# Kernel optimization log

Hardware: AMD Instinct MI355X
Metric: run time of the kernel (lower is better)

The kernel has to match this reference:

```python
import jax, jax.numpy as jnp
import numpy as np

B, IN, OUT = 8192, 1024, 1024


def setup_inputs() -> dict:
    key = jax.random.key(0)
    k1, k2 = jax.random.split(key)
    x = jax.random.normal(k1, (B, IN), dtype=jnp.float32)
    W_seed = jax.random.normal(k2, (IN, OUT), dtype=jnp.float32) / np.sqrt(IN).astype(np.float32)
    b_seed = jnp.zeros((OUT,), dtype=jnp.float32)
    W_sig = jnp.zeros((2,), dtype=jnp.float32)  # mixture logits over ['dense','Toeplitz']
    b_sig = jnp.zeros((2,), dtype=jnp.float32)  # mixture logits over ['dense','None']
    A_sig = jnp.zeros((2,), dtype=jnp.float32)  # mixture logits over ['linear','relu']
    return {"x": x, "W_seed": W_seed, "b_seed": b_seed,
            "W_sig": W_sig, "b_sig": b_sig, "A_sig": A_sig}


def _toeplitz_from_seed(W_seed):
    # seed_vec = [W_seed[0, out-1], ..., W_seed[0, 1], W_seed[0,0], ..., W_seed[in-1,0]]
    in_sz, out_sz = W_seed.shape
    seed_vec = jnp.concatenate([W_seed[0, -1:0:-1], W_seed[:, 0]])  # [out-1 + in]
    # W_toep[i, j] = seed_vec[i - j + out - 1]
    idx = jnp.arange(in_sz)[:, None] - jnp.arange(out_sz)[None, :] + (out_sz - 1)
    return seed_vec[idx]  # [in, out]


def reference(x, W_seed, b_seed, W_sig, b_sig, A_sig):
    W_toep = _toeplitz_from_seed(W_seed)
    w_s = jax.nn.softmax(W_sig)
    W_core = w_s[0] * W_seed + w_s[1] * W_toep          # softmax-weighted weight mixture
    b_s = jax.nn.softmax(b_sig)
    b_core = b_s[0] * b_seed                             # 'None' branch contributes zeros
    out = x @ W_core + b_core                            # [B, out]
    a_s = jax.nn.softmax(A_sig)
    return a_s[0] * out + a_s[1] * jax.nn.relu(out)      # activation mixture
```

## Files before the change

### kernel.cpp

```cpp
#include <hip/hip_runtime.h>

typedef unsigned short ushort_t;
typedef __bf16 bf16x8 __attribute__((ext_vector_type(8)));
typedef float f32x4 __attribute__((ext_vector_type(4)));

#define AS1 __attribute__((address_space(1)))
#define AS3 __attribute__((address_space(3)))

__device__ __forceinline__ ushort_t f2bf(float f) {
    unsigned u = __builtin_bit_cast(unsigned, f);
    u = (u + 0x7fffu + ((u >> 16) & 1u)) >> 16;
    return (ushort_t)u;
}

__device__ __forceinline__ void async16(void* lds, const void* g) {
    __builtin_amdgcn_global_load_lds((const AS1 unsigned int*)g,
                                     (AS3 unsigned int*)lds, 16, 0, 0);
}

__device__ __forceinline__ void softmax2(const float* __restrict__ sig, float& s0, float& s1) {
    float a = sig[0], b = sig[1];
    float m = fmaxf(a, b);
    float e0 = __expf(a - m), e1 = __expf(b - m);
    float inv = 1.0f / (e0 + e1);
    s0 = e0 * inv; s1 = e1 * inv;
}

__device__ __forceinline__ float toep_val(const float* __restrict__ Wseed, int k, int o) {
    return (k >= o) ? Wseed[(size_t)(k - o) << 10] : Wseed[o - k];
}

__global__ __launch_bounds__(256) void prep_w_kernel(const float* __restrict__ Wseed,
                                                     const float* __restrict__ Wsig,
                                                     ushort_t* __restrict__ Wt) {
    __shared__ float T[64][65];
    int bb = blockIdx.x;
    int k0 = (bb >> 4) * 64;
    int o0 = (bb & 15) * 64;
    int t = threadIdx.x;
    #pragma unroll
    for (int i = 0; i < 4; ++i) {
        int lin = t + i * 256;
        int kr = lin >> 4;
        int c4 = lin & 15;
        float4 v = *(const float4*)&Wseed[(size_t)(k0 + kr) * 1024 + o0 + c4 * 4];
        T[kr][c4 * 4 + 0] = v.x;
        T[kr][c4 * 4 + 1] = v.y;
        T[kr][c4 * 4 + 2] = v.z;
        T[kr][c4 * 4 + 3] = v.w;
    }
    __syncthreads();
    float s0, s1; softmax2(Wsig, s0, s1);
    #pragma unroll
    for (int i = 0; i < 2; ++i) {
        int lin = t + i * 256;
        int oo = lin >> 3;
        int kq = (lin & 7) * 8;
        unsigned r[4];
        #pragma unroll
        for (int q = 0; q < 4; ++q) {
            float v0 = s0 * T[kq + 2 * q + 0][oo] + s1 * toep_val(Wseed, k0 + kq + 2 * q + 0, o0 + oo);
            float v1 = s0 * T[kq + 2 * q + 1][oo] + s1 * toep_val(Wseed, k0 + kq + 2 * q + 1, o0 + oo);
            r[q] = (unsigned)f2bf(v0) | ((unsigned)f2bf(v1) << 16);
        }
        *(uint4*)&Wt[(size_t)(o0 + oo) * 1024 + k0 + kq] = make_uint4(r[0], r[1], r[2], r[3]);
    }
}

#define BM 128
#define BN 128
#define BK 32
#define NKT 32

__global__ __launch_bounds__(512, 2) void gemm_kernel(const float* __restrict__ Xf,
                                                      const ushort_t* __restrict__ Wt,
                                                      const float* __restrict__ bseed,
                                                      const float* __restrict__ bsig,
                                                      const float* __restrict__ asig,
                                                      float* __restrict__ out) {
    __shared__ ushort_t lds[24576];
    ushort_t* At0 = lds;
    ushort_t* Bt0 = lds + 8192;
    ushort_t* At1 = lds + 12288;
    ushort_t* Bt1 = lds + 20480;

    const int t = threadIdx.x;
    const int wv = t >> 6;
    const int lane = t & 63;

    const int orig = blockIdx.x;
    const int g = orig & 7;
    const int within = orig >> 3;
    const int rb = g * 8 + (within >> 3);
    const int cb = within & 7;
    const int brow = rb * BM;
    const int bcol = cb * BN;

    const int ra = t >> 3;
    const int ca = (t & 7) ^ (ra & 7);
    const float* gAsw = Xf + (size_t)(brow + ra) * 1024 + 4 * ca;

    const int rbb = t >> 2;
    const int cbk = (t & 3) ^ (rbb & 3);
    const ushort_t* gBsw = Wt + (size_t)(bcol + rbb) * 1024 + 8 * cbk;

    f32x4 acc[2][4];
    #pragma unroll
    for (int i = 0; i < 2; ++i)
        #pragma unroll
        for (int j = 0; j < 4; ++j) acc[i][j] = (f32x4){0.f, 0.f, 0.f, 0.f};

    const int wr = (wv >> 1) * 32;
    const int wcn = (wv & 1) * 64;
    const int fr = lane & 15;
    const int kg = (lane >> 4) * 8;
    const int c0 = (lane >> 4) * 2;

    float bs0, bs1, as0, as1;
    softmax2(bsig, bs0, bs1);
    softmax2(asig, as0, as1);
    float bias[4];
    #pragma unroll
    for (int ni = 0; ni < 4; ++ni)
        bias[ni] = bs0 * bseed[bcol + wcn + ni * 16 + fr];
    asm volatile("" :: "v"(bias[0]), "v"(bias[1]), "v"(bias[2]), "v"(bias[3]),
                       "v"(as0), "v"(as1));
    asm volatile("" ::: "memory");

#define STAGEA(Abuf, ko)                                           \
    do {                                                           \
        async16((Abuf) + wv * 512,        gAsw + (ko));            \
        async16((Abuf) + 4096 + wv * 512, gAsw + 65536 + (ko));    \
    } while (0)

#define STAGEB(Bbuf, ko)                                   \
    do {                                                   \
        async16((Bbuf) + wv * 512, gBsw + (ko));           \
    } while (0)

#define COMPUTE(Abuf, Bbuf)                                                        \
    do {                                                                           \
        const float* Af_ = (const float*)(Abuf);                                   \
        bf16x8 af[2], bf[4];                                                       \
        _Pragma("unroll")                                                          \
        for (int mi = 0; mi < 2; ++mi) {                                           \
            int row_ = wr + mi * 16 + fr;                                          \
            f32x4 lo_ = *(const f32x4*)&Af_[row_ * 32 + (((c0)     ^ (row_ & 7)) << 2)]; \
            f32x4 hi_ = *(const f32x4*)&Af_[row_ * 32 + (((c0 + 1) ^ (row_ & 7)) << 2)]; \
            bf16x8 a_;                                                             \
            _Pragma("unroll")                                                      \
            for (int j_ = 0; j_ < 4; ++j_) {                                       \
                a_[j_]     = (__bf16)lo_[j_];                                      \
                a_[4 + j_] = (__bf16)hi_[j_];                                      \
            }                                                                      \
            af[mi] = a_;                                                           \
        }                                                                          \
        _Pragma("unroll")                                                          \
        for (int ni = 0; ni < 4; ++ni) {                                           \
            int rb_ = wcn + ni * 16 + fr;                                          \
            int ch_ = ((kg >> 3) ^ (rb_ & 3)) << 3;                                \
            bf[ni] = *(const bf16x8*)&(Bbuf)[rb_ * 32 + ch_];                      \
        }                                                                          \
        _Pragma("unroll")                                                          \
        for (int mi = 0; mi < 2; ++mi)                                             \
            _Pragma("unroll")                                                      \
            for (int ni = 0; ni < 4; ++ni)                                         \
                acc[mi][ni] = __builtin_amdgcn_mfma_f32_16x16x32_bf16(             \
                    af[mi], bf[ni], acc[mi][ni], 0, 0, 0);                         \
    } while (0)

#define SYNC() do { asm volatile("s_waitcnt vmcnt(0) lgkmcnt(0)" ::: "memory");    \
                    __builtin_amdgcn_s_barrier(); } while (0)

    STAGEA(At0, 0);
    STAGEB(Bt0, 0);
    SYNC();
    for (int it = 0; it < 15; ++it) {
        STAGEA(At1, (2 * it + 1) * BK);
        STAGEB(Bt1, (2 * it + 1) * BK);
        COMPUTE(At0, Bt0);
        SYNC();
        STAGEA(At0, (2 * it + 2) * BK);
        STAGEB(Bt0, (2 * it + 2) * BK);
        COMPUTE(At1, Bt1);
        SYNC();
    }
    STAGEA(At1, 31 * BK);
    STAGEB(Bt1, 31 * BK);
    COMPUTE(At0, Bt0);
    SYNC();
    COMPUTE(At1, Bt1);

    #pragma unroll
    for (int ni = 0; ni < 4; ++ni) {
        int col = bcol + wcn + ni * 16 + fr;
        #pragma unroll
        for (int mi = 0; mi < 2; ++mi) {
            int row = brow + wr + mi * 16 + (lane >> 4) * 4;
            #pragma unroll
            for (int r = 0; r < 4; ++r) {
                float v = acc[mi][ni][r] + bias[ni];
                out[(size_t)(row + r) * 1024 + col] = as0 * v + as1 * fmaxf(v, 0.f);
            }
        }
    }
#undef STAGEA
#undef STAGEB
#undef COMPUTE
#undef SYNC
}

__global__ __launch_bounds__(256) void naive_kernel(const float* __restrict__ x,
                                                    const float* __restrict__ Wseed,
                                                    const float* __restrict__ bseed,
                                                    const float* __restrict__ Wsig,
                                                    const float* __restrict__ bsig,
                                                    const float* __restrict__ asig,
                                                    float* __restrict__ out) {
    int idx = blockIdx.x * 256 + threadIdx.x;
    int b = idx >> 10, o = idx & 1023;
    float ws0, ws1, bs0, bs1, as0, as1;
    softmax2(Wsig, ws0, ws1);
    softmax2(bsig, bs0, bs1);
    softmax2(asig, as0, as1);
    float s = 0.f;
    const float* xr = x + (size_t)b * 1024;
    for (int k = 0; k < 1024; ++k) {
        float wc = ws0 * Wseed[((size_t)k << 10) + o] + ws1 * toep_val(Wseed, k, o);
        s += xr[k] * wc;
    }
    float v = s + bs0 * bseed[o];
    out[idx] = as0 * v + as1 * fmaxf(v, 0.f);
}

extern "C" void kernel_launch(void* const* d_in, const int* in_sizes, int n_in,
                              void* d_out, int out_size, void* d_ws, size_t ws_size,
                              hipStream_t stream) {
    const float* x     = (const float*)d_in[0];
    const float* Wseed = (const float*)d_in[1];
    const float* bseed = (const float*)d_in[2];
    const float* Wsig  = (const float*)d_in[3];
    const float* bsig  = (const float*)d_in[4];
    const float* Asig  = (const float*)d_in[5];
    float* out = (float*)d_out;

    const size_t need = (2u << 20) + 1024;
    if (ws_size < need) {
        naive_kernel<<<dim3(8192 * 1024 / 256), dim3(256), 0, stream>>>(
            x, Wseed, bseed, Wsig, bsig, Asig, out);
        return;
    }

    ushort_t* Wt = (ushort_t*)d_ws;

    prep_w_kernel<<<dim3(256), dim3(256), 0, stream>>>(Wseed, Wsig, Wt);
    gemm_kernel<<<dim3(512), dim3(512), 0, stream>>>(x, Wt, bseed, bsig, Asig, out);
}
```

Before: 38.84 us.

## Use triple-buffered LDS pipeline with partial vmcnt waits in GEMM

Replaces the double-buffered A/B staging with a three-stage rotating LDS buffer, so loads for tile T+2 are issued while tile T is computed. Waits use a partial vmcnt so only the oldest stage must land before each barrier. The B-tile XOR swizzle now keys on (row>>1) to change the LDS bank pattern, and the launch bounds request 4 blocks per CU. The risks are higher LDS use (72KB per block), which limits occupancy, and register pressure under the tighter launch bound.

New measurement: 39.18 us. About the same (+0.9%).

```diff
diff --git a/kernel.cpp b/kernel.cpp
--- a/kernel.cpp
+++ b/kernel.cpp
@@ -72,17 +72,16 @@
 #define BK 32
 #define NKT 32
 
-__global__ __launch_bounds__(512, 2) void gemm_kernel(const float* __restrict__ Xf,
+__global__ __launch_bounds__(512, 4) void gemm_kernel(const float* __restrict__ Xf,
                                                       const ushort_t* __restrict__ Wt,
                                                       const float* __restrict__ bseed,
                                                       const float* __restrict__ bsig,
                                                       const float* __restrict__ asig,
                                                       float* __restrict__ out) {
-    __shared__ ushort_t lds[24576];
-    ushort_t* At0 = lds;
-    ushort_t* Bt0 = lds + 8192;
-    ushort_t* At1 = lds + 12288;
-    ushort_t* Bt1 = lds + 20480;
+    __shared__ ushort_t lds[36864];
+    ushort_t* p0 = lds;
+    ushort_t* p1 = lds + 12288;
+    ushort_t* p2 = lds + 24576;
 
     const int t = threadIdx.x;
     const int wv = t >> 6;
@@ -101,7 +100,7 @@
     const float* gAsw = Xf + (size_t)(brow + ra) * 1024 + 4 * ca;
 
     const int rbb = t >> 2;
-    const int cbk = (t & 3) ^ (rbb & 3);
+    const int cbk = (t & 3) ^ ((rbb >> 1) & 3);
     const ushort_t* gBsw = Wt + (size_t)(bcol + rbb) * 1024 + 8 * cbk;
 
     f32x4 acc[2][4];
@@ -127,20 +126,16 @@
                        "v"(as0), "v"(as1));
     asm volatile("" ::: "memory");
 
-#define STAGEA(Abuf, ko)                                           \
+#define STAGE(buf, ko)                                             \
     do {                                                           \
-        async16((Abuf) + wv * 512,        gAsw + (ko));            \
-        async16((Abuf) + 4096 + wv * 512, gAsw + 65536 + (ko));    \
+        async16((buf) + wv * 512,        gAsw + (ko));             \
+        async16((buf) + 4096 + wv * 512, gAsw + 65536 + (ko));     \
+        async16((buf) + 8192 + wv * 512, gBsw + (ko));             \
     } while (0)
 
-#define STAGEB(Bbuf, ko)                                   \
-    do {                                                   \
-        async16((Bbuf) + wv * 512, gBsw + (ko));           \
-    } while (0)
-
-#define COMPUTE(Abuf, Bbuf)                                                        \
+#define COMPUTE(buf)                                                               \
     do {                                                                           \
-        const float* Af_ = (const float*)(Abuf);                                   \
+        const float* Af_ = (const float*)(buf);                                    \
         bf16x8 af[2], bf[4];                                                       \
         _Pragma("unroll")                                                          \
         for (int mi = 0; mi < 2; ++mi) {                                           \
@@ -158,8 +153,8 @@
         _Pragma("unroll")                                                          \
         for (int ni = 0; ni < 4; ++ni) {                                           \
             int rb_ = wcn + ni * 16 + fr;                                          \
-            int ch_ = ((kg >> 3) ^ (rb_ & 3)) << 3;                                \
-            bf[ni] = *(const bf16x8*)&(Bbuf)[rb_ * 32 + ch_];                      \
+            int ch_ = ((kg >> 3) ^ ((rb_ >> 1) & 3)) << 3;                         \
+            bf[ni] = *(const bf16x8*)&(buf)[8192 + rb_ * 32 + ch_];                \
         }                                                                          \
         _Pragma("unroll")                                                          \
         for (int mi = 0; mi < 2; ++mi)                                             \
@@ -169,27 +164,20 @@
                     af[mi], bf[ni], acc[mi][ni], 0, 0, 0);                         \
     } while (0)
 
-#define SYNC() do { asm volatile("s_waitcnt vmcnt(0) lgkmcnt(0)" ::: "memory");    \
-                    __builtin_amdgcn_s_barrier(); } while (0)
-
-    STAGEA(At0, 0);
-    STAGEB(Bt0, 0);
-    SYNC();
-    for (int it = 0; it < 15; ++it) {
-        STAGEA(At1, (2 * it + 1) * BK);
-        STAGEB(Bt1, (2 * it + 1) * BK);
-        COMPUTE(At0, Bt0);
-        SYNC();
-        STAGEA(At0, (2 * it + 2) * BK);
-        STAGEB(Bt0, (2 * it + 2) * BK);
-        COMPUTE(At1, Bt1);
-        SYNC();
-    }
-    STAGEA(At1, 31 * BK);
-    STAGEB(Bt1, 31 * BK);
-    COMPUTE(At0, Bt0);
-    SYNC();
-    COMPUTE(At1, Bt1);
+    STAGE(p0, 0);
+    STAGE(p1, BK);
+    asm volatile("s_waitcnt vmcnt(3)" ::: "memory");
+    __builtin_amdgcn_s_barrier();
+
+    for (int T = 0; T < NKT; ++T) {
+        if (T + 2 < NKT) STAGE(p2, (size_t)(T + 2) * BK);
+        COMPUTE(p0);
+        if (T < NKT - 2)       { asm volatile("s_waitcnt vmcnt(3)" ::: "memory");
+                                 __builtin_amdgcn_s_barrier(); }
+        else if (T == NKT - 2) { asm volatile("s_waitcnt vmcnt(0)" ::: "memory");
+                                 __builtin_amdgcn_s_barrier(); }
+        ushort_t* tmp_ = p0; p0 = p1; p1 = p2; p2 = tmp_;
+    }
 
     #pragma unroll
     for (int ni = 0; ni < 4; ++ni) {
@@ -204,10 +192,8 @@
             }
         }
     }
-#undef STAGEA
-#undef STAGEB
+#undef STAGE
 #undef COMPUTE
-#undef SYNC
 }
 
 __global__ __launch_bounds__(256) void naive_kernel(const float* __restrict__ x,
```
